# Kernel tuning notes

Measured on AMD Instinct MI355X. Metric: run time of the kernel, lower is better.

## Reference

```python
import jax, jax.numpy as jnp
import numpy as np

N_QUBITS = 10
N_LAYERS = 4
DIM = 2 ** N_QUBITS  # 1024
IN_FEATURES = 512
OUT_FEATURES = 64
BATCH = 4096


def setup_inputs() -> dict:
    key = jax.random.key(0)
    ks = jax.random.split(key, 6)
    return {
        "x": jax.random.normal(ks[0], (BATCH, IN_FEATURES), dtype=jnp.float32),
        "W_pre": jax.random.normal(ks[1], (DIM, IN_FEATURES), dtype=jnp.float32) / np.float32(np.sqrt(IN_FEATURES)),
        "b_pre": jnp.zeros((DIM,), dtype=jnp.float32),
        "q_weights": jax.random.normal(ks[2], (N_LAYERS, N_QUBITS, 3), dtype=jnp.float32),
        "W_post": jax.random.normal(ks[3], (OUT_FEATURES, N_QUBITS), dtype=jnp.float32) / np.float32(np.sqrt(N_QUBITS)),
        "b_post": jnp.zeros((OUT_FEATURES,), dtype=jnp.float32),
    }


def _rot_matrices(w):
    # w: [L, n, 3] -> PennyLane Rot(phi, theta, omega) = RZ(omega) RY(theta) RZ(phi)
    phi, theta, omega = w[..., 0], w[..., 1], w[..., 2]
    c = jnp.cos(theta / 2).astype(jnp.complex64)
    s = jnp.sin(theta / 2).astype(jnp.complex64)
    e_mm = jnp.exp(-0.5j * (phi + omega))
    e_pp = jnp.exp(0.5j * (phi + omega))
    e_pm = jnp.exp(0.5j * (phi - omega))
    e_mp = jnp.exp(-0.5j * (phi - omega))
    row0 = jnp.stack([e_mm * c, -e_pm * s], axis=-1)
    row1 = jnp.stack([e_mp * s, e_pp * c], axis=-1)
    return jnp.stack([row0, row1], axis=-2)  # [L, n, 2, 2] complex64


def _apply_1q(psi, U, wire):
    # psi: [B, 2, 2, ..., 2]; apply 2x2 unitary U on qubit `wire` (axis wire+1)
    axis = wire + 1
    psi = jnp.moveaxis(psi, axis, -1)
    psi = psi @ U.T  # new[a] = sum_b U[a,b] psi[b]
    return jnp.moveaxis(psi, -1, axis)


def _cnot(psi, control, target):
    ca, ta = control + 1, target + 1
    p0 = jax.lax.index_in_dim(psi, 0, ca, keepdims=True)
    p1 = jax.lax.index_in_dim(psi, 1, ca, keepdims=True)
    p1 = jnp.flip(p1, axis=ta)  # flip target amplitudes where control = 1
    return jnp.concatenate([p0, p1], axis=ca)


def _quantum_forward(amps, q_weights):
    # AmplitudeEmbedding(normalize=True) + StronglyEntanglingLayers + PauliZ expvals, batched.
    B = amps.shape[0]
    norm = jnp.sqrt(jnp.sum(amps * amps, axis=1, keepdims=True))
    psi = (amps / norm).astype(jnp.complex64).reshape((B,) + (2,) * N_QUBITS)
    U = _rot_matrices(q_weights)
    for l in range(N_LAYERS):
        for w in range(N_QUBITS):
            psi = _apply_1q(psi, U[l, w], w)
        r = (l % (N_QUBITS - 1)) + 1  # PennyLane default ranges
        for w in range(N_QUBITS):
            psi = _cnot(psi, w, (w + r) % N_QUBITS)
    probs = psi.real ** 2 + psi.imag ** 2
    axes_all = tuple(range(1, N_QUBITS + 1))
    z = []
    for i in range(N_QUBITS):
        other = tuple(a for a in axes_all if a != i + 1)
        marg = jnp.sum(probs, axis=other)  # [B, 2]
        z.append(marg[:, 0] - marg[:, 1])
    return jnp.stack(z, axis=1)  # [B, n_qubits]


def reference(x, W_pre, b_pre, q_weights, W_post, b_post):
    h = jax.nn.relu(x @ W_pre.T + b_pre)          # [B, 2^n]
    z = _quantum_forward(h, q_weights)            # [B, n_qubits]
    return z @ W_post.T + b_post                  # [B, out_features]
```

## Files before the change

kernel.cpp:

```cpp
#include <hip/hip_runtime.h>
#include <hip/hip_bf16.h>
#include <math.h>

#define NQ   10
#define DIM  1024
#define NL   4
#define INF  512
#define OUTF 64
#define MBATCH 4096

typedef _Float16 half8 __attribute__((ext_vector_type(8)));
typedef float f32x4 __attribute__((ext_vector_type(4)));
typedef float f32x2 __attribute__((ext_vector_type(2)));

#define WS_H16  0
#define WS_ROT  (8u * 1024u * 1024u)
#define WS_TAB  (8u * 1024u * 1024u + 4096u)

#define HD __host__ __device__

HD constexpr int fstep(int j, int r) {
    for (int w2 = NQ - 1; w2 >= 0; --w2) {
        const int cb = 9 - w2;
        const int tb = 9 - ((w2 + r) % NQ);
        j ^= ((j >> cb) & 1) << tb;
    }
    return j;
}
HD constexpr int ifstep(int j, int r) {
    for (int w2 = 0; w2 < NQ; ++w2) {
        const int cb = 9 - w2;
        const int tb = 9 - ((w2 + r) % NQ);
        j ^= ((j >> cb) & 1) << tb;
    }
    return j;
}
HD constexpr int sigma_fwd(int l, int x) {
    for (int t = l - 1; t >= 0; --t) x = fstep(x, t + 1);
    return x;
}
HD constexpr int sigma_inv(int l, int s) {
    for (int t = 0; t < l; ++t) s = ifstep(s, t + 1);
    return s;
}
constexpr int gate_m(int l, int b) { return sigma_fwd(l, 1 << b); }
constexpr int gate_g(int l, int b) {
    int g = 0;
    for (int j = 0; j < NQ; ++j)
        if ((sigma_inv(l, 1 << j) >> b) & 1) g |= 1 << j;
    return g;
}
struct QM { int v[NQ]; };
constexpr QM make_qm() {
    QM q{};
    for (int w = 0; w < NQ; ++w) {
        const int B = 9 - w;
        int m = 0;
        for (int j = 0; j < NQ; ++j)
            if ((sigma_inv(NL, 1 << j) >> B) & 1) m |= 1 << j;
        q.v[w] = m;
    }
    return q;
}
constexpr QM QMASKS = make_qm();

constexpr int mask_at(int t) { return gate_m(t / 10, 9 - (t % 10)); }
constexpr int pick_wbit() {
    int best = 9, bc = 1000;
    for (int j = 3; j <= 9; ++j) {
        int c = 0;
        for (int t = 0; t < 40; ++t) c += (mask_at(t) >> j) & 1;
        if (c < bc) { bc = c; best = j; }
    }
    return best;
}
constexpr int WBIT = pick_wbit();
struct LP { int v[6]; };
constexpr LP make_lpos() {
    LP p{}; int n = 0;
    for (int j = 3; j <= 9; ++j) if (j != WBIT) p.v[n++] = j;
    return p;
}
constexpr LP LPOS = make_lpos();
constexpr int lx_extract(int m) {
    int r = 0;
    for (int t = 0; t < 6; ++t) if ((m >> LPOS.v[t]) & 1) r |= 1 << t;
    return r;
}

__global__ __launch_bounds__(256) void setup_kernel(
    const float* __restrict__ qw, float2* __restrict__ rot,
    float2* __restrict__ tabs)
{
    const int tid = threadIdx.x;
    if (tid < NL * NQ) {
        float s, c; sincosf(0.5f * qw[tid * 3 + 1], &s, &c);
        rot[tid] = float2{c, s};
    }
    for (int u = 0; u < 4; ++u) {
        const int s_ = (tid << 2) + u;
        float a = 0.f;
        for (int w = 0; w < NQ; ++w)
            a += qw[w * 3 + 0] * (((s_ >> (9 - w)) & 1) ? 1.f : -1.f);
        float si, co; sincosf(0.5f * a, &si, &co);
        tabs[s_] = float2{co, si};
        for (int l = 0; l < 3; ++l) {
            const int j  = sigma_inv(l, s_);
            const int ip = sigma_inv(l + 1, s_);
            float b = 0.f;
            for (int w = 0; w < NQ; ++w) {
                b += qw[(l * NQ + w) * 3 + 2]       * (((j  >> (9 - w)) & 1) ? 1.f : -1.f);
                b += qw[((l + 1) * NQ + w) * 3 + 0] * (((ip >> (9 - w)) & 1) ? 1.f : -1.f);
            }
            sincosf(0.5f * b, &si, &co);
            tabs[(l + 1) * DIM + s_] = float2{co, si};
        }
    }
}

__global__ __launch_bounds__(256) void gemm_kernel(
    const float* __restrict__ X, const float* __restrict__ W,
    const float* __restrict__ bias, _Float16* __restrict__ H)
{
    constexpr int BM = 128, BN = 64, BK = 32, LDP = BK + 8;
    __shared__ _Float16 As[BM][LDP];
    __shared__ _Float16 Bs[BN][LDP];

    const int tid = threadIdx.x;
    const int wave = tid >> 6, lane = tid & 63;
    const int wm = wave >> 1, wn = wave & 1;
    const int l15 = lane & 15, lk = (lane >> 4) * 8;

    const int arow = tid >> 1, ahalf = tid & 1;
    const int brow = tid & 63, bseg = tid >> 6;

    const float* ag = X + (size_t)(blockIdx.x * BM + arow) * INF + ahalf * 16;
    const float* bg = W + (size_t)(blockIdx.y * BN + brow) * INF + bseg * 8;

    f32x4 acc[4][2] = {};

    for (int k0 = 0; k0 < INF; k0 += BK) {
        float4 a0 = *reinterpret_cast<const float4*>(ag + k0);
        float4 a1 = *reinterpret_cast<const float4*>(ag + k0 + 4);
        float4 a2 = *reinterpret_cast<const float4*>(ag + k0 + 8);
        float4 a3 = *reinterpret_cast<const float4*>(ag + k0 + 12);
        float4 b0 = *reinterpret_cast<const float4*>(bg + k0);
        float4 b1 = *reinterpret_cast<const float4*>(bg + k0 + 4);
        half8 ha0 = {(_Float16)a0.x, (_Float16)a0.y, (_Float16)a0.z, (_Float16)a0.w,
                     (_Float16)a1.x, (_Float16)a1.y, (_Float16)a1.z, (_Float16)a1.w};
        half8 ha1 = {(_Float16)a2.x, (_Float16)a2.y, (_Float16)a2.z, (_Float16)a2.w,
                     (_Float16)a3.x, (_Float16)a3.y, (_Float16)a3.z, (_Float16)a3.w};
        half8 hb  = {(_Float16)b0.x, (_Float16)b0.y, (_Float16)b0.z, (_Float16)b0.w,
                     (_Float16)b1.x, (_Float16)b1.y, (_Float16)b1.z, (_Float16)b1.w};
        __syncthreads();
        *reinterpret_cast<half8*>(&As[arow][ahalf * 16])     = ha0;
        *reinterpret_cast<half8*>(&As[arow][ahalf * 16 + 8]) = ha1;
        *reinterpret_cast<half8*>(&Bs[brow][bseg * 8])       = hb;
        __syncthreads();
        half8 bfr0 = *reinterpret_cast<const half8*>(&Bs[wn * 32 + l15][lk]);
        half8 bfr1 = *reinterpret_cast<const half8*>(&Bs[wn * 32 + 16 + l15][lk]);
#pragma unroll
        for (int mi = 0; mi < 4; ++mi) {
            half8 afr = *reinterpret_cast<const half8*>(&As[wm * 64 + mi * 16 + l15][lk]);
            acc[mi][0] = __builtin_amdgcn_mfma_f32_16x16x32_f16(afr, bfr0, acc[mi][0], 0, 0, 0);
            acc[mi][1] = __builtin_amdgcn_mfma_f32_16x16x32_f16(afr, bfr1, acc[mi][1], 0, 0, 0);
        }
    }

    const int crow0 = blockIdx.x * BM + wm * 64;
    const int ccol0 = blockIdx.y * BN + wn * 32;
#pragma unroll
    for (int ni = 0; ni < 2; ++ni) {
        const int col = ccol0 + ni * 16 + l15;
        const float bb = bias[col];
#pragma unroll
        for (int mi = 0; mi < 4; ++mi) {
#pragma unroll
            for (int r = 0; r < 4; ++r) {
                const int row = crow0 + mi * 16 + (lane >> 4) * 4 + r;
                const float o = fmaxf(acc[mi][ni][r] + bb, 0.f);
                H[(size_t)row * DIM + col] = (_Float16)o;
            }
        }
    }
}

template<int MHI>
__device__ __forceinline__ int lxi(int v, int lane) {
    if constexpr (MHI == 0)
        return v;
    else if constexpr (MHI == 1)
        return __builtin_amdgcn_mov_dpp(v, 0xB1, 0xF, 0xF, false);
    else if constexpr (MHI == 2)
        return __builtin_amdgcn_mov_dpp(v, 0x4E, 0xF, 0xF, false);
    else if constexpr (MHI == 3)
        return __builtin_amdgcn_mov_dpp(v, 0x1B, 0xF, 0xF, false);
    else if constexpr (MHI == 8)
        return __builtin_amdgcn_mov_dpp(v, 0x128, 0xF, 0xF, false);
    else if constexpr (MHI < 32)
        return __builtin_amdgcn_ds_swizzle(v, 0x1F | (MHI << 10));
    else
        return __builtin_amdgcn_ds_bpermute((lane ^ MHI) << 2, v);
}

template<int MHI>
__device__ __forceinline__ float lxf(float v, int lane) {
    return __int_as_float(lxi<MHI>(__float_as_int(v), lane));
}

__device__ __forceinline__ float allred(float v, int lane) {
    v += lxf<1>(v, lane);
    v += lxf<2>(v, lane);
    v += lxf<4>(v, lane);
    v += lxf<8>(v, lane);
    v += lxf<16>(v, lane);
    v += lxf<32>(v, lane);
    return v;
}

template<int L, int W>
__device__ __forceinline__ void apply_ry(f32x2 rr[4], f32x2 ii[4],
                                         const float2* __restrict__ rot,
                                         int lane, int wave,
                                         f32x4 (*buf)[2][64])
{
    constexpr int b = 9 - W;
    constexpr int m = gate_m(L, b);
    constexpr int g = gate_g(L, b);
    constexpr int MW    = (m >> WBIT) & 1;
    constexpr int MLANE = lx_extract(m);
    constexpr int MREG  = m & 7;
    constexpr int GW    = (g >> WBIT) & 1;
    constexpr int GLANE = lx_extract(g);
    constexpr int GREG  = g & 7;

    const float2 cs = rot[L * NQ + W];
    int hli = __builtin_popcount(lane & GLANE) & 1;
    if constexpr (GW) hli ^= wave;
    const float sp = hli ? cs.y : -cs.y;
    const float sn = -sp;
    const f32x2 C = {cs.x, cs.x};

    float pr[8], pi[8];
    if constexpr (MW == 0) {
#pragma unroll
        for (int k = 0; k < 8; ++k) {
            const int kp = k ^ MREG;
            const float vr = (kp & 1) ? rr[kp >> 1].y : rr[kp >> 1].x;
            const float vi = (kp & 1) ? ii[kp >> 1].y : ii[kp >> 1].x;
            pr[k] = lxf<MLANE>(vr, lane);
            pi[k] = lxf<MLANE>(vi, lane);
        }
    } else {
        buf[0][wave][lane] = f32x4{rr[0].x, rr[0].y, rr[1].x, rr[1].y};
        buf[1][wave][lane] = f32x4{rr[2].x, rr[2].y, rr[3].x, rr[3].y};
        buf[2][wave][lane] = f32x4{ii[0].x, ii[0].y, ii[1].x, ii[1].y};
        buf[3][wave][lane] = f32x4{ii[2].x, ii[2].y, ii[3].x, ii[3].y};
        __syncthreads();
        const int pl = lane ^ MLANE;
        const int pw = wave ^ 1;
        const f32x4 R0 = buf[0][pw][pl];
        const f32x4 R1 = buf[1][pw][pl];
        const f32x4 I0 = buf[2][pw][pl];
        const f32x4 I1 = buf[3][pw][pl];
        __syncthreads();
#pragma unroll
        for (int k = 0; k < 8; ++k) {
            const int kp = k ^ MREG;
            pr[k] = (kp & 4) ? R1[kp & 3] : R0[kp & 3];
            pi[k] = (kp & 4) ? I1[kp & 3] : I0[kp & 3];
        }
    }
#pragma unroll
    for (int j = 0; j < 4; ++j) {
        const int k0 = 2 * j, k1 = 2 * j + 1;
        const float s0 = (__builtin_popcount(k0 & GREG) & 1) ? sn : sp;
        const float s1 = (__builtin_popcount(k1 & GREG) & 1) ? sn : sp;
        const f32x2 S = {s0, s1};
        const f32x2 PR = {pr[k0], pr[k1]};
        const f32x2 PI = {pi[k0], pi[k1]};
        rr[j] = C * rr[j] + S * PR;
        ii[j] = C * ii[j] + S * PI;
    }
}

__device__ __forceinline__ void apply_diag(f32x2 rr[4], f32x2 ii[4],
                                           const f32x4* __restrict__ q)
{
#pragma unroll
    for (int j = 0; j < 4; ++j) {
        const f32x4 v = q[j];
        const f32x2 CR = {v.x, v.z};
        const f32x2 CI = {v.y, v.w};
        const f32x2 R = rr[j], I = ii[j];
        rr[j] = R * CR - I * CI;
        ii[j] = I * CR + R * CI;
    }
}

template<int L>
__device__ __forceinline__ void apply_layer(f32x2 rr[4], f32x2 ii[4],
                                            const float2* __restrict__ rot,
                                            int lane, int wave,
                                            f32x4 (*buf)[2][64])
{
    apply_ry<L, 0>(rr, ii, rot, lane, wave, buf);
    apply_ry<L, 1>(rr, ii, rot, lane, wave, buf);
    apply_ry<L, 2>(rr, ii, rot, lane, wave, buf);
    apply_ry<L, 3>(rr, ii, rot, lane, wave, buf);
    apply_ry<L, 4>(rr, ii, rot, lane, wave, buf);
    apply_ry<L, 5>(rr, ii, rot, lane, wave, buf);
    apply_ry<L, 6>(rr, ii, rot, lane, wave, buf);
    apply_ry<L, 7>(rr, ii, rot, lane, wave, buf);
    apply_ry<L, 8>(rr, ii, rot, lane, wave, buf);
    apply_ry<L, 9>(rr, ii, rot, lane, wave, buf);
}

__global__ __launch_bounds__(128, 8) void quantum_kernel(
    const _Float16* __restrict__ Hbuf, const float2* __restrict__ rot,
    const float2* __restrict__ tabs, const float* __restrict__ W_post,
    const float* __restrict__ b_post, float* __restrict__ out)
{
    __shared__ f32x4 buf[4][2][64];
    __shared__ float sred[34];

    const int lane = threadIdx.x;
    const int wave = threadIdx.y;
    const int row  = blockIdx.x;

    int pb = wave << WBIT;
#pragma unroll
    for (int t = 0; t < 6; ++t) pb |= ((lane >> t) & 1) << LPOS.v[t];

    const _Float16* hr = Hbuf + (size_t)row * DIM + pb;
    f32x2 A[4];
    {
        half8 h0 = *reinterpret_cast<const half8*>(hr);
#pragma unroll
        for (int j = 0; j < 4; ++j)
            A[j] = f32x2{(float)h0[2 * j], (float)h0[2 * j + 1]};
    }

    f32x2 n2 = f32x2{0.f, 0.f};
#pragma unroll
    for (int j = 0; j < 4; ++j) n2 += A[j] * A[j];
    float nw = allred(n2.x + n2.y, lane);
    if (lane == 0) sred[32 + wave] = nw;
    __syncthreads();
    const float inv_nrm = 1.0f / (sred[32] + sred[33]);

    f32x2 rr[4], ii[4];
    {
        const f32x4* q = reinterpret_cast<const f32x4*>(tabs + pb);
#pragma unroll
        for (int j = 0; j < 4; ++j) {
            const f32x4 v = q[j];
            rr[j] = A[j] * f32x2{v.x, v.z};
            ii[j] = A[j] * f32x2{v.y, v.w};
        }
    }

    apply_layer<0>(rr, ii, rot, lane, wave, buf);
    apply_diag(rr, ii, reinterpret_cast<const f32x4*>(tabs + 1 * DIM + pb));
    apply_layer<1>(rr, ii, rot, lane, wave, buf);
    apply_diag(rr, ii, reinterpret_cast<const f32x4*>(tabs + 2 * DIM + pb));
    apply_layer<2>(rr, ii, rot, lane, wave, buf);
    apply_diag(rr, ii, reinterpret_cast<const f32x4*>(tabs + 3 * DIM + pb));
    apply_layer<3>(rr, ii, rot, lane, wave, buf);

    f32x2 P[4];
#pragma unroll
    for (int j = 0; j < 4; ++j) P[j] = rr[j] * rr[j] + ii[j] * ii[j];

    float z[NQ];
#pragma unroll
    for (int w = 0; w < NQ; ++w) {
        const int q = QMASKS.v[w];
        const int qw_ = (q >> WBIT) & 1;
        const int qlane = lx_extract(q);
        const int qreg = q & 7;
        float zl = 0.f;
#pragma unroll
        for (int j = 0; j < 4; ++j) {
            const float s0 = (__builtin_popcount((2 * j) & qreg) & 1) ? -1.f : 1.f;
            const float s1 = (__builtin_popcount((2 * j + 1) & qreg) & 1) ? -1.f : 1.f;
            zl += s0 * P[j].x + s1 * P[j].y;
        }
        int neg = __builtin_popcount(lane & qlane) & 1;
        neg ^= (wave & qw_);
        if (neg) zl = -zl;
        z[w] = allred(zl, lane);
    }
    if (lane == 0) {
#pragma unroll
        for (int w = 0; w < NQ; ++w) sred[wave * 16 + w] = z[w];
    }
    __syncthreads();

    if (wave == 0) {
        float o = b_post[lane];
#pragma unroll
        for (int w = 0; w < NQ; ++w)
            o = fmaf((sred[w] + sred[16 + w]) * inv_nrm, W_post[lane * NQ + w], o);
        out[(size_t)row * OUTF + lane] = o;
    }
}

extern "C" void kernel_launch(void* const* d_in, const int* in_sizes, int n_in,
                              void* d_out, int out_size, void* d_ws, size_t ws_size,
                              hipStream_t stream) {
    const float* x      = (const float*)d_in[0];
    const float* W_pre  = (const float*)d_in[1];
    const float* b_pre  = (const float*)d_in[2];
    const float* qw     = (const float*)d_in[3];
    const float* W_post = (const float*)d_in[4];
    const float* b_post = (const float*)d_in[5];
    float* out = (float*)d_out;

    char* ws = (char*)d_ws;
    _Float16* h16 = (_Float16*)(ws + WS_H16);
    float2*   rot = (float2*)  (ws + WS_ROT);
    float2*   tabs= (float2*)  (ws + WS_TAB);

    setup_kernel<<<1, 256, 0, stream>>>(qw, rot, tabs);
    dim3 g1(MBATCH / 128, DIM / 64);
    gemm_kernel<<<g1, 256, 0, stream>>>(x, W_pre, b_pre, h16);
    quantum_kernel<<<MBATCH, dim3(64, 2), 0, stream>>>(h16, rot, tabs, W_post, b_post, out);
}
```

Measured before the change: 70.73 us.

## Pre-convert GEMM inputs to fp16 in setup kernel and prefetch diagonal tables

Adds a conversion pass to the setup kernel that writes fp16 copies of x and W_pre to workspace. The GEMM then reads half-precision operands directly instead of loading fp32 and converting inside the K loop, which halves the bytes it re-reads across tiles. The quantum kernel also loads each layer's diagonal phase table into registers before the layer runs, so the global-load latency overlaps with the rotation work. The cost is an extra fp32 read plus fp16 write pass over x and W and more register pressure in the quantum kernel.

```diff
diff --git a/kernel.cpp b/kernel.cpp
--- a/kernel.cpp
+++ b/kernel.cpp
@@ -14,8 +14,10 @@
 typedef float f32x2 __attribute__((ext_vector_type(2)));
 
 #define WS_H16  0
-#define WS_ROT  (8u * 1024u * 1024u)
-#define WS_TAB  (8u * 1024u * 1024u + 4096u)
+#define WS_X16  (8u * 1024u * 1024u)
+#define WS_W16  (12u * 1024u * 1024u)
+#define WS_ROT  (13u * 1024u * 1024u)
+#define WS_TAB  (13u * 1024u * 1024u + 4096u)
 
 #define HD __host__ __device__
 
@@ -89,37 +91,56 @@
 }
 
 __global__ __launch_bounds__(256) void setup_kernel(
-    const float* __restrict__ qw, float2* __restrict__ rot,
+    const float* __restrict__ x, const float* __restrict__ w,
+    const float* __restrict__ qw, _Float16* __restrict__ x16,
+    _Float16* __restrict__ w16, float2* __restrict__ rot,
     float2* __restrict__ tabs)
 {
+    const int bid = blockIdx.x;
     const int tid = threadIdx.x;
-    if (tid < NL * NQ) {
-        float s, c; sincosf(0.5f * qw[tid * 3 + 1], &s, &c);
-        rot[tid] = float2{c, s};
-    }
-    for (int u = 0; u < 4; ++u) {
-        const int s_ = (tid << 2) + u;
-        float a = 0.f;
-        for (int w = 0; w < NQ; ++w)
-            a += qw[w * 3 + 0] * (((s_ >> (9 - w)) & 1) ? 1.f : -1.f);
-        float si, co; sincosf(0.5f * a, &si, &co);
-        tabs[s_] = float2{co, si};
-        for (int l = 0; l < 3; ++l) {
-            const int j  = sigma_inv(l, s_);
-            const int ip = sigma_inv(l + 1, s_);
-            float b = 0.f;
-            for (int w = 0; w < NQ; ++w) {
-                b += qw[(l * NQ + w) * 3 + 2]       * (((j  >> (9 - w)) & 1) ? 1.f : -1.f);
-                b += qw[((l + 1) * NQ + w) * 3 + 0] * (((ip >> (9 - w)) & 1) ? 1.f : -1.f);
+    if (bid < 1024) {
+        const int base = bid * 2048 + tid * 8;
+        float4 a = *reinterpret_cast<const float4*>(x + base);
+        float4 b = *reinterpret_cast<const float4*>(x + base + 4);
+        half8 o = {(_Float16)a.x, (_Float16)a.y, (_Float16)a.z, (_Float16)a.w,
+                   (_Float16)b.x, (_Float16)b.y, (_Float16)b.z, (_Float16)b.w};
+        *reinterpret_cast<half8*>(x16 + base) = o;
+    } else if (bid < 1280) {
+        const int base = (bid - 1024) * 2048 + tid * 8;
+        float4 a = *reinterpret_cast<const float4*>(w + base);
+        float4 b = *reinterpret_cast<const float4*>(w + base + 4);
+        half8 o = {(_Float16)a.x, (_Float16)a.y, (_Float16)a.z, (_Float16)a.w,
+                   (_Float16)b.x, (_Float16)b.y, (_Float16)b.z, (_Float16)b.w};
+        *reinterpret_cast<half8*>(w16 + base) = o;
+    } else {
+        if (tid < NL * NQ) {
+            float s, c; sincosf(0.5f * qw[tid * 3 + 1], &s, &c);
+            rot[tid] = float2{c, s};
+        }
+        for (int u = 0; u < 4; ++u) {
+            const int s_ = (tid << 2) + u;
+            float a = 0.f;
+            for (int w2 = 0; w2 < NQ; ++w2)
+                a += qw[w2 * 3 + 0] * (((s_ >> (9 - w2)) & 1) ? 1.f : -1.f);
+            float si, co; sincosf(0.5f * a, &si, &co);
+            tabs[s_] = float2{co, si};
+            for (int l = 0; l < 3; ++l) {
+                const int j  = sigma_inv(l, s_);
+                const int ip = sigma_inv(l + 1, s_);
+                float b = 0.f;
+                for (int w2 = 0; w2 < NQ; ++w2) {
+                    b += qw[(l * NQ + w2) * 3 + 2]       * (((j  >> (9 - w2)) & 1) ? 1.f : -1.f);
+                    b += qw[((l + 1) * NQ + w2) * 3 + 0] * (((ip >> (9 - w2)) & 1) ? 1.f : -1.f);
+                }
+                sincosf(0.5f * b, &si, &co);
+                tabs[(l + 1) * DIM + s_] = float2{co, si};
             }
-            sincosf(0.5f * b, &si, &co);
-            tabs[(l + 1) * DIM + s_] = float2{co, si};
-        }
-    }
-}
-
-__global__ __launch_bounds__(256) void gemm_kernel(
-    const float* __restrict__ X, const float* __restrict__ W,
+        }
+    }
+}
+
+__global__ __launch_bounds__(256) void gemm16_kernel(
+    const _Float16* __restrict__ X, const _Float16* __restrict__ W,
     const float* __restrict__ bias, _Float16* __restrict__ H)
 {
     constexpr int BM = 128, BN = 64, BK = 32, LDP = BK + 8;
@@ -134,28 +155,19 @@
     const int arow = tid >> 1, ahalf = tid & 1;
     const int brow = tid & 63, bseg = tid >> 6;
 
-    const float* ag = X + (size_t)(blockIdx.x * BM + arow) * INF + ahalf * 16;
-    const float* bg = W + (size_t)(blockIdx.y * BN + brow) * INF + bseg * 8;
+    const _Float16* ag = X + (size_t)(blockIdx.x * BM + arow) * INF + ahalf * 16;
+    const _Float16* bg = W + (size_t)(blockIdx.y * BN + brow) * INF + bseg * 8;
 
     f32x4 acc[4][2] = {};
 
     for (int k0 = 0; k0 < INF; k0 += BK) {
-        float4 a0 = *reinterpret_cast<const float4*>(ag + k0);
-        float4 a1 = *reinterpret_cast<const float4*>(ag + k0 + 4);
-        float4 a2 = *reinterpret_cast<const float4*>(ag + k0 + 8);
-        float4 a3 = *reinterpret_cast<const float4*>(ag + k0 + 12);
-        float4 b0 = *reinterpret_cast<const float4*>(bg + k0);
-        float4 b1 = *reinterpret_cast<const float4*>(bg + k0 + 4);
-        half8 ha0 = {(_Float16)a0.x, (_Float16)a0.y, (_Float16)a0.z, (_Float16)a0.w,
-                     (_Float16)a1.x, (_Float16)a1.y, (_Float16)a1.z, (_Float16)a1.w};
-        half8 ha1 = {(_Float16)a2.x, (_Float16)a2.y, (_Float16)a2.z, (_Float16)a2.w,
-                     (_Float16)a3.x, (_Float16)a3.y, (_Float16)a3.z, (_Float16)a3.w};
-        half8 hb  = {(_Float16)b0.x, (_Float16)b0.y, (_Float16)b0.z, (_Float16)b0.w,
-                     (_Float16)b1.x, (_Float16)b1.y, (_Float16)b1.z, (_Float16)b1.w};
+        half8 av0 = *reinterpret_cast<const half8*>(ag + k0);
+        half8 av1 = *reinterpret_cast<const half8*>(ag + k0 + 8);
+        half8 bv  = *reinterpret_cast<const half8*>(bg + k0);
         __syncthreads();
-        *reinterpret_cast<half8*>(&As[arow][ahalf * 16])     = ha0;
-        *reinterpret_cast<half8*>(&As[arow][ahalf * 16 + 8]) = ha1;
-        *reinterpret_cast<half8*>(&Bs[brow][bseg * 8])       = hb;
+        *reinterpret_cast<half8*>(&As[arow][ahalf * 16])     = av0;
+        *reinterpret_cast<half8*>(&As[arow][ahalf * 16 + 8]) = av1;
+        *reinterpret_cast<half8*>(&Bs[brow][bseg * 8])       = bv;
         __syncthreads();
         half8 bfr0 = *reinterpret_cast<const half8*>(&Bs[wn * 32 + l15][lk]);
         half8 bfr1 = *reinterpret_cast<const half8*>(&Bs[wn * 32 + 16 + l15][lk]);
@@ -284,14 +296,13 @@
     }
 }
 
-__device__ __forceinline__ void apply_diag(f32x2 rr[4], f32x2 ii[4],
-                                           const f32x4* __restrict__ q)
+__device__ __forceinline__ void apply_diag_reg(f32x2 rr[4], f32x2 ii[4],
+                                               const f32x4 d[4])
 {
 #pragma unroll
     for (int j = 0; j < 4; ++j) {
-        const f32x4 v = q[j];
-        const f32x2 CR = {v.x, v.z};
-        const f32x2 CI = {v.y, v.w};
+        const f32x2 CR = {d[j].x, d[j].z};
+        const f32x2 CI = {d[j].y, d[j].w};
         const f32x2 R = rr[j], I = ii[j];
         rr[j] = R * CR - I * CI;
         ii[j] = I * CR + R * CI;
@@ -332,13 +343,21 @@
 #pragma unroll
     for (int t = 0; t < 6; ++t) pb |= ((lane >> t) & 1) << LPOS.v[t];
 
+    const f32x4* t0 = reinterpret_cast<const f32x4*>(tabs + pb);
+    const f32x4* t1 = reinterpret_cast<const f32x4*>(tabs + 1 * DIM + pb);
+    const f32x4* t2 = reinterpret_cast<const f32x4*>(tabs + 2 * DIM + pb);
+    const f32x4* t3 = reinterpret_cast<const f32x4*>(tabs + 3 * DIM + pb);
+
     const _Float16* hr = Hbuf + (size_t)row * DIM + pb;
     f32x2 A[4];
+    f32x4 d[4];
     {
         half8 h0 = *reinterpret_cast<const half8*>(hr);
 #pragma unroll
-        for (int j = 0; j < 4; ++j)
+        for (int j = 0; j < 4; ++j) {
             A[j] = f32x2{(float)h0[2 * j], (float)h0[2 * j + 1]};
+            d[j] = t0[j];
+        }
     }
 
     f32x2 n2 = f32x2{0.f, 0.f};
@@ -350,22 +369,24 @@
     const float inv_nrm = 1.0f / (sred[32] + sred[33]);
 
     f32x2 rr[4], ii[4];
-    {
-        const f32x4* q = reinterpret_cast<const f32x4*>(tabs + pb);
-#pragma unroll
-        for (int j = 0; j < 4; ++j) {
-            const f32x4 v = q[j];
-            rr[j] = A[j] * f32x2{v.x, v.z};
-            ii[j] = A[j] * f32x2{v.y, v.w};
-        }
-    }
-
+#pragma unroll
+    for (int j = 0; j < 4; ++j) {
+        rr[j] = A[j] * f32x2{d[j].x, d[j].z};
+        ii[j] = A[j] * f32x2{d[j].y, d[j].w};
+    }
+
+#pragma unroll
+    for (int j = 0; j < 4; ++j) d[j] = t1[j];
     apply_layer<0>(rr, ii, rot, lane, wave, buf);
-    apply_diag(rr, ii, reinterpret_cast<const f32x4*>(tabs + 1 * DIM + pb));
+    apply_diag_reg(rr, ii, d);
+#pragma unroll
+    for (int j = 0; j < 4; ++j) d[j] = t2[j];
     apply_layer<1>(rr, ii, rot, lane, wave, buf);
-    apply_diag(rr, ii, reinterpret_cast<const f32x4*>(tabs + 2 * DIM + pb));
+    apply_diag_reg(rr, ii, d);
+#pragma unroll
+    for (int j = 0; j < 4; ++j) d[j] = t3[j];
     apply_layer<2>(rr, ii, rot, lane, wave, buf);
-    apply_diag(rr, ii, reinterpret_cast<const f32x4*>(tabs + 3 * DIM + pb));
+    apply_diag_reg(rr, ii, d);
     apply_layer<3>(rr, ii, rot, lane, wave, buf);
 
     f32x2 P[4];
@@ -419,11 +440,13 @@
 
     char* ws = (char*)d_ws;
     _Float16* h16 = (_Float16*)(ws + WS_H16);
+    _Float16* x16 = (_Float16*)(ws + WS_X16);
+    _Float16* w16 = (_Float16*)(ws + WS_W16);
     float2*   rot = (float2*)  (ws + WS_ROT);
     float2*   tabs= (float2*)  (ws + WS_TAB);
 
-    setup_kernel<<<1, 256, 0, stream>>>(qw, rot, tabs);
+    setup_kernel<<<1281, 256, 0, stream>>>(x, W_pre, qw, x16, w16, rot, tabs);
     dim3 g1(MBATCH / 128, DIM / 64);
-    gemm_kernel<<<g1, 256, 0, stream>>>(x, W_pre, b_pre, h16);
+    gemm16_kernel<<<g1, 256, 0, stream>>>(x16, w16, b_pre, h16);
     quantum_kernel<<<MBATCH, dim3(64, 2), 0, stream>>>(h16, rot, tabs, W_post, b_post, out);
 }
```

Measured after the change: 65.05 us. -8.0%, faster.
